# Optimization experiments

Measured on AMD Instinct MI355X. Metric: run time of the kernel, lower is better.

Reference implementation:

```python
import jax, jax.numpy as jnp
import numpy as np

N_HEAD = 16
HEAD_DIM = 64

def setup_inputs() -> dict:
    key = jax.random.key(0)
    k1, k2, k3 = jax.random.split(key, 3)
    B, S, D = 4, 2048, 1024
    x = jax.random.normal(k1, (B, S, D), dtype=jnp.float32)
    mask = jnp.tril(jnp.ones((S, S), dtype=bool))[None, None]  # (1,1,S,S) causal
    w_attn = jax.random.normal(k2, (D, 3 * D), dtype=jnp.float32) * (1.0 / np.sqrt(D))
    b_attn = jnp.zeros((3 * D,), dtype=jnp.float32)
    w_proj = jax.random.normal(k3, (D, D), dtype=jnp.float32) * (1.0 / np.sqrt(D))
    b_proj = jnp.zeros((D,), dtype=jnp.float32)
    return {"x": x, "mask": mask, "w_attn": w_attn, "b_attn": b_attn,
            "w_proj": w_proj, "b_proj": b_proj}

def reference(x, mask, w_attn, b_attn, w_proj, b_proj):
    B, S, D = x.shape
    H, hd = N_HEAD, HEAD_DIM
    qkv = x @ w_attn + b_attn                      # (B,S,3D)
    q, k, v = jnp.split(qkv, 3, axis=-1)
    q = q.reshape(B, S, H, hd).transpose(0, 2, 1, 3)  # (B,H,S,hd)
    k = k.reshape(B, S, H, hd).transpose(0, 2, 1, 3)
    v = v.reshape(B, S, H, hd).transpose(0, 2, 1, 3)
    scores = jnp.einsum('bhqd,bhkd->bhqk', q, k) / jnp.sqrt(jnp.float32(hd))
    scores = jnp.where(mask, scores, jnp.float32(-1e10))
    weights = jax.nn.softmax(scores, axis=-1)      # dropout is identity (deterministic=True)
    attn = jnp.einsum('bhqk,bhkd->bhqd', weights, v)
    attn = attn.transpose(0, 2, 1, 3).reshape(B, S, D)
    return attn @ w_proj + b_proj
```

## Files before the change

### kernel.cpp

```cpp
#include <hip/hip_runtime.h>
#include <hip/hip_bf16.h>
#include <stdint.h>


typedef uint16_t u16;
typedef __bf16 bf16x8 __attribute__((ext_vector_type(8)));
typedef __bf16 bf16x4 __attribute__((ext_vector_type(4)));
typedef short s16x4 __attribute__((ext_vector_type(4)));
typedef float f32x4 __attribute__((ext_vector_type(4)));

#define S_LEN 2048
#define DMODEL 1024
#define NHEAD 16
#define HDIM 64
#define MTOT 8192
#define NQKV 3072

__device__ __forceinline__ u16 f2bf(float f) {
    union { float f; uint32_t u; } v; v.f = f;
    uint32_t u = v.u;
    return (u16)((u + 0x7fffu + ((u >> 16) & 1u)) >> 16);
}

__device__ __forceinline__ s16x4 bits4(bf16x4 v) {
    union { bf16x4 b; s16x4 s; } u; u.b = v; return u.s;
}

__device__ __forceinline__ f32x4 mfma16(bf16x4 a, bf16x4 b, f32x4 c) {
    return __builtin_amdgcn_mfma_f32_16x16x16bf16_1k(bits4(a), bits4(b), c, 0, 0, 0);
}

__device__ __forceinline__ void async_load16(const void* g, void* l) {
    __builtin_amdgcn_global_load_lds(
        (__attribute__((address_space(1))) void*)g,
        (__attribute__((address_space(3))) void*)l,
        16, 0, 0);
}

__global__ void convert_x_kernel(const float4* __restrict__ in, ushort4* __restrict__ out, int n4) {
    int i = blockIdx.x * 256 + threadIdx.x;
    if (i < n4) {
        float4 f = in[i];
        ushort4 o;
        o.x = f2bf(f.x); o.y = f2bf(f.y); o.z = f2bf(f.z); o.w = f2bf(f.w);
        out[i] = o;
    }
}

__global__ void transpose_bf16_kernel(const float* __restrict__ in, u16* __restrict__ out, int R, int C) {
    __shared__ float tile[64][65];
    int r0 = blockIdx.y * 64, c0 = blockIdx.x * 64;
    #pragma unroll
    for (int i = 0; i < 16; ++i) {
        int idx = threadIdx.x + i * 256;
        int r = idx >> 6, c = idx & 63;
        tile[r][c] = in[(size_t)(r0 + r) * C + c0 + c];
    }
    __syncthreads();
    #pragma unroll
    for (int i = 0; i < 16; ++i) {
        int idx = threadIdx.x + i * 256;
        int c = idx >> 6, r = idx & 63;
        out[(size_t)(c0 + c) * R + r0 + r] = f2bf(tile[r][c]);
    }
}

__global__ void transpose_v_kernel(const u16* __restrict__ qkv, u16* __restrict__ vt) {
    __shared__ u16 tile[64 * 66];
    const int tid = threadIdx.x;
    const int stile = blockIdx.x, bh = blockIdx.y;
    const int b = bh >> 4, h = bh & 15;
    const u16* src = qkv + ((size_t)b * S_LEN + stile * 64) * NQKV + 2 * DMODEL + h * HDIM;
    #pragma unroll
    for (int it = 0; it < 2; ++it) {
        int item = it * 256 + tid;
        int s = item >> 3, d0 = (item & 7) * 8;
        bf16x8 v = *(const bf16x8*)(src + (size_t)s * NQKV + d0);
        const u16* vu = (const u16*)&v;
        #pragma unroll
        for (int j = 0; j < 8; ++j) tile[(d0 + j) * 66 + s] = vu[j];
    }
    __syncthreads();
    #pragma unroll
    for (int it = 0; it < 2; ++it) {
        int item = it * 256 + tid;
        int d = item >> 3, s0 = (item & 7) * 8;
        union { u16 u[8]; uint4 v; } pk;
        #pragma unroll
        for (int j = 0; j < 8; ++j) pk.u[j] = tile[d * 66 + s0 + j];
        *(uint4*)(vt + ((size_t)bh * 64 + d) * S_LEN + stile * 64 + s0) = pk.v;
    }
}

template<bool OUT_BF16>
__global__ __launch_bounds__(512, 2) void gemm256(
    const u16* __restrict__ A, const u16* __restrict__ Bt,
    const float* __restrict__ bias, void* __restrict__ C,
    int M, int N, int K)
{
    __shared__ __attribute__((aligned(16))) u16 sm[49152];
    const int tid = threadIdx.x;
    const int wave = tid >> 6, lane = tid & 63;
    const int l15 = lane & 15, q4 = lane >> 4;
    const int wm = wave & 3, wn = wave >> 2;

    const int bid = (int)blockIdx.x;
    const int xcd = bid & 7;
    const int l   = bid >> 3;
    const int MB  = M >> 8;
    const int PM  = MB >> 3;
    const int nb  = l / PM;
    const int mb  = xcd * PM + (l - nb * PM);
    const int m0 = mb << 8, n0 = nb << 7;

    const u16* Ag = A + (size_t)m0 * K;
    const u16* Bg = Bt + (size_t)n0 * K;

    const int srow = tid >> 3;
    const size_t goff0 = (size_t)srow * K + (size_t)(((tid & 7) ^ (srow & 7)) * 8);
    const size_t goff1 = goff0 + (size_t)64 * K;
    const int ldso = tid * 8;

    const int ck0 = (q4 ^ (l15 & 7)) * 8;
    const int ck1 = ((4 + q4) ^ (l15 & 7)) * 8;
    const int ra0 = (wm * 32 + l15) * 64;
    const int ra1 = ra0 + 16 * 64;
    const int rb0 = (wn * 64 + l15) * 64;

    f32x4 acc[4][4] = {};
    const int T = K >> 6;

    u16* const As = sm;
    u16* const Bs = sm + 32768;

    {
        async_load16(Ag + goff0, As + ldso);
        async_load16(Ag + goff1, As + ldso + 4096);
        async_load16(Bg + goff0, Bs + ldso);
        async_load16(Bg + goff1, Bs + ldso + 4096);
        async_load16(Ag + (size_t)128 * K + goff0, As + 8192 + ldso);
        async_load16(Ag + (size_t)128 * K + goff1, As + 8192 + ldso + 4096);
        if (T > 1) {
            async_load16(Ag + 64 + goff0, As + 2 * 8192 + ldso);
            async_load16(Ag + 64 + goff1, As + 2 * 8192 + ldso + 4096);
            async_load16(Bg + 64 + goff0, Bs + 8192 + ldso);
            async_load16(Bg + 64 + goff1, Bs + 8192 + ldso + 4096);
            asm volatile("s_waitcnt vmcnt(4)" ::: "memory");
        } else {
            asm volatile("s_waitcnt vmcnt(0)" ::: "memory");
        }
        asm volatile("s_barrier" ::: "memory");
    }

    for (int t = 0; t < T; ++t) {
        const int par = t & 1;
        const u16* As0 = As + par * 2 * 8192;
        const u16* As1 = As0 + 8192;
        const u16* Bsl = Bs + par * 8192;

        bf16x8 bfr[4][2], afr[2][2];
        #pragma unroll
        for (int nf = 0; nf < 4; ++nf) {
            bfr[nf][0] = *(const bf16x8*)(Bsl + rb0 + nf * (16 * 64) + ck0);
            bfr[nf][1] = *(const bf16x8*)(Bsl + rb0 + nf * (16 * 64) + ck1);
        }
        afr[0][0] = *(const bf16x8*)(As0 + ra0 + ck0);
        afr[0][1] = *(const bf16x8*)(As0 + ra0 + ck1);
        afr[1][0] = *(const bf16x8*)(As0 + ra1 + ck0);
        afr[1][1] = *(const bf16x8*)(As0 + ra1 + ck1);
        if (t + 1 < T) {
            const u16* g = Ag + (size_t)128 * K + (size_t)(t + 1) * 64;
            u16* l2 = As + ((par ^ 1) * 2 + 1) * 8192;
            async_load16(g + goff0, l2 + ldso);
            async_load16(g + goff1, l2 + ldso + 4096);
        }
        asm volatile("s_barrier" ::: "memory");
        __builtin_amdgcn_s_setprio(1);
        #pragma unroll
        for (int m = 0; m < 2; ++m)
            #pragma unroll
            for (int nf = 0; nf < 4; ++nf)
                #pragma unroll
                for (int kk = 0; kk < 2; ++kk)
                    acc[m][nf] = __builtin_amdgcn_mfma_f32_16x16x32_bf16(
                        afr[m][kk], bfr[nf][kk], acc[m][nf], 0, 0, 0);
        __builtin_amdgcn_s_setprio(0);
        asm volatile("s_barrier" ::: "memory");

        afr[0][0] = *(const bf16x8*)(As1 + ra0 + ck0);
        afr[0][1] = *(const bf16x8*)(As1 + ra0 + ck1);
        afr[1][0] = *(const bf16x8*)(As1 + ra1 + ck0);
        afr[1][1] = *(const bf16x8*)(As1 + ra1 + ck1);
        if (t + 2 < T) {
            const u16* ga = Ag + (size_t)(t + 2) * 64;
            const u16* gb = Bg + (size_t)(t + 2) * 64;
            u16* la = As + par * 2 * 8192;
            u16* lb = Bs + par * 8192;
            async_load16(ga + goff0, la + ldso);
            async_load16(ga + goff1, la + ldso + 4096);
            async_load16(gb + goff0, lb + ldso);
            async_load16(gb + goff1, lb + ldso + 4096);
        }
        asm volatile("s_barrier" ::: "memory");
        __builtin_amdgcn_s_setprio(1);
        #pragma unroll
        for (int m = 0; m < 2; ++m)
            #pragma unroll
            for (int nf = 0; nf < 4; ++nf)
                #pragma unroll
                for (int kk = 0; kk < 2; ++kk)
                    acc[2 + m][nf] = __builtin_amdgcn_mfma_f32_16x16x32_bf16(
                        afr[m][kk], bfr[nf][kk], acc[2 + m][nf], 0, 0, 0);
        __builtin_amdgcn_s_setprio(0);
        if (t + 1 < T) {
            if (t + 2 < T) asm volatile("s_waitcnt vmcnt(4)" ::: "memory");
            else           asm volatile("s_waitcnt vmcnt(0)" ::: "memory");
            asm volatile("s_barrier" ::: "memory");
        }
    }

    #pragma unroll
    for (int mf = 0; mf < 4; ++mf) {
        const int row = m0 + (mf >> 1) * 128 + wm * 32 + (mf & 1) * 16 + q4 * 4;
        #pragma unroll
        for (int nf = 0; nf < 4; ++nf) {
            const int col = n0 + wn * 64 + nf * 16 + l15;
            const float bv = bias[col];
            #pragma unroll
            for (int r = 0; r < 4; ++r) {
                float v = acc[mf][nf][r] + bv;
                if (OUT_BF16) ((u16*)C)[(size_t)(row + r) * N + col] = f2bf(v);
                else          ((float*)C)[(size_t)(row + r) * N + col] = v;
            }
        }
    }
}

__device__ __forceinline__ void stage_tiles(
    const u16* __restrict__ qkv, const u16* __restrict__ vt,
    size_t base, int bh, int h, int w, int srow8, int schunk,
    int kt, u16* __restrict__ KsB, u16* __restrict__ VsB)
{
    #pragma unroll
    for (int q = 0; q < 2; ++q) {
        int rloc = w * 16 + q * 8 + srow8;
        int sc = ((schunk ^ (rloc & 7)) * 8);
        async_load16(qkv + (base + (size_t)kt * 64 + rloc) * (size_t)NQKV + DMODEL + h * HDIM + sc,
                     KsB + (w * 16 + q * 8) * 64);
        async_load16(vt + ((size_t)bh * 64 + rloc) * S_LEN + kt * 64 + sc,
                     VsB + (w * 16 + q * 8) * 64);
    }
}

__device__ __forceinline__ void attn_pass(
    int qt, const u16* __restrict__ qkv, const u16* __restrict__ vt,
    __bf16* __restrict__ outb, u16 (*Ks)[64 * 64], u16 (*Vs)[64 * 64],
    int w, int lane, int bh, int h, size_t base)
{
    const int l15 = lane & 15, q4 = lane >> 4;
    const int srow8 = lane >> 3, schunk = lane & 7;

    const float QSCALE = 0.125f * 1.44269504f;
    bf16x8 qf[2][2];
    #pragma unroll
    for (int mh = 0; mh < 2; ++mh) {
        int qrow = qt * 128 + mh * 64 + w * 16 + l15;
        #pragma unroll
        for (int kc = 0; kc < 2; ++kc) {
            bf16x8 raw = *(const bf16x8*)(qkv + (base + qrow) * (size_t)NQKV + h * HDIM + kc * 32 + q4 * 8);
            bf16x8 sc;
            #pragma unroll
            for (int j = 0; j < 8; ++j) sc[j] = (__bf16)((float)raw[j] * QSCALE);
            qf[mh][kc] = sc;
        }
    }

    bf16x4 ones4;
    #pragma unroll
    for (int j = 0; j < 4; ++j) ones4[j] = (__bf16)1.0f;

    f32x4 o0[4] = {}, o1[4] = {};
    f32x4 la0 = {}, la1 = {};

    const int ktlast = 2 * qt + 1;

    __syncthreads();
    stage_tiles(qkv, vt, base, bh, h, w, srow8, schunk, 0, Ks[0], Vs[0]);
    if (ktlast >= 1)
        stage_tiles(qkv, vt, base, bh, h, w, srow8, schunk, 1, Ks[1], Vs[1]);

    for (int kt = 0; kt <= 2 * qt; ++kt) {
        const int buf = kt % 3;
        __syncthreads();
        int pf = kt + 2;
        if (pf <= ktlast)
            stage_tiles(qkv, vt, base, bh, h, w, srow8, schunk, pf, Ks[pf % 3], Vs[pf % 3]);

        f32x4 st0[4] = {}, st1[4] = {};
        #pragma unroll
        for (int nt = 0; nt < 4; ++nt) {
            int n = nt * 16 + l15;
            #pragma unroll
            for (int kc = 0; kc < 2; ++kc) {
                int ch = (((kc * 4 + q4) ^ (n & 7)) * 8);
                bf16x8 kf = *(const bf16x8*)(&Ks[buf][n * 64 + ch]);
                st0[nt] = __builtin_amdgcn_mfma_f32_16x16x32_bf16(kf, qf[0][kc], st0[nt], 0, 0, 0);
                st1[nt] = __builtin_amdgcn_mfma_f32_16x16x32_bf16(kf, qf[1][kc], st1[nt], 0, 0, 0);
            }
        }

        if (kt == 2 * qt) {
            #pragma unroll
            for (int nt = 0; nt < 4; ++nt)
                #pragma unroll
                for (int r = 0; r < 4; ++r) {
                    int keyl = nt * 16 + q4 * 4 + r;
                    if (keyl > w * 16 + l15) st0[nt][r] = -1e30f;
                }
        }

        bf16x4 pb0[4], pb1[4];
        #pragma unroll
        for (int nt = 0; nt < 4; ++nt)
            #pragma unroll
            for (int r = 0; r < 4; ++r) {
                pb0[nt][r] = (__bf16)__builtin_amdgcn_exp2f(st0[nt][r]);
                pb1[nt][r] = (__bf16)__builtin_amdgcn_exp2f(st1[nt][r]);
            }

        #pragma unroll
        for (int nt = 0; nt < 4; ++nt) {
            #pragma unroll
            for (int mt = 0; mt < 4; ++mt) {
                int row = mt * 16 + l15;
                int ch = (nt * 2 + (q4 >> 1)) ^ (row & 7);
                bf16x4 vf = *(const bf16x4*)(&Vs[buf][row * 64 + ch * 8 + (q4 & 1) * 4]);
                o0[mt] = mfma16(vf, pb0[nt], o0[mt]);
                o1[mt] = mfma16(vf, pb1[nt], o1[mt]);
            }
            la0 = mfma16(ones4, pb0[nt], la0);
            la1 = mfma16(ones4, pb1[nt], la1);
        }
    }

    {
        const int buf = ktlast % 3;
        __syncthreads();

        f32x4 st1[4] = {};
        #pragma unroll
        for (int nt = 0; nt < 4; ++nt) {
            int n = nt * 16 + l15;
            #pragma unroll
            for (int kc = 0; kc < 2; ++kc) {
                int ch = (((kc * 4 + q4) ^ (n & 7)) * 8);
                bf16x8 kf = *(const bf16x8*)(&Ks[buf][n * 64 + ch]);
                st1[nt] = __builtin_amdgcn_mfma_f32_16x16x32_bf16(kf, qf[1][kc], st1[nt], 0, 0, 0);
            }
        }
        bf16x4 pb1[4];
        #pragma unroll
        for (int nt = 0; nt < 4; ++nt)
            #pragma unroll
            for (int r = 0; r < 4; ++r) {
                int keyl = nt * 16 + q4 * 4 + r;
                float s = (keyl > w * 16 + l15) ? -1e30f : st1[nt][r];
                pb1[nt][r] = (__bf16)__builtin_amdgcn_exp2f(s);
            }
        #pragma unroll
        for (int nt = 0; nt < 4; ++nt) {
            #pragma unroll
            for (int mt = 0; mt < 4; ++mt) {
                int row = mt * 16 + l15;
                int ch = (nt * 2 + (q4 >> 1)) ^ (row & 7);
                bf16x4 vf = *(const bf16x4*)(&Vs[buf][row * 64 + ch * 8 + (q4 & 1) * 4]);
                o1[mt] = mfma16(vf, pb1[nt], o1[mt]);
            }
            la1 = mfma16(ones4, pb1[nt], la1);
        }
    }

    float inv0 = 1.0f / la0[0], inv1 = 1.0f / la1[0];
    int row0 = qt * 128 + w * 16 + l15;
    int row1 = row0 + 64;
    #pragma unroll
    for (int mt = 0; mt < 4; ++mt) {
        union { __bf16 b[4]; ushort4 v; } p0, p1;
        #pragma unroll
        for (int r = 0; r < 4; ++r) {
            p0.b[r] = (__bf16)(o0[mt][r] * inv0);
            p1.b[r] = (__bf16)(o1[mt][r] * inv1);
        }
        int col = h * HDIM + mt * 16 + q4 * 4;
        *(ushort4*)(&outb[(base + row0) * (size_t)DMODEL + col]) = p0.v;
        *(ushort4*)(&outb[(base + row1) * (size_t)DMODEL + col]) = p1.v;
    }
}

__global__ __launch_bounds__(256, 3) void attn_kernel(
    const u16* __restrict__ qkv, const u16* __restrict__ vt, u16* __restrict__ out)
{
    __shared__ __attribute__((aligned(16))) u16 Ks[3][64 * 64];
    __shared__ __attribute__((aligned(16))) u16 Vs[3][64 * 64];

    const int tid = threadIdx.x;
    const int w = tid >> 6, lane = tid & 63;
    const int bh = blockIdx.y;
    const int b = bh >> 4, h = bh & 15;
    const size_t base = (size_t)b * S_LEN;
    const int NT = (int)gridDim.x * 2;

    attn_pass(NT - 1 - (int)blockIdx.x, qkv, vt, (__bf16*)out, Ks, Vs, w, lane, bh, h, base);
    attn_pass((int)blockIdx.x,          qkv, vt, (__bf16*)out, Ks, Vs, w, lane, bh, h, base);
}

extern "C" void kernel_launch(void* const* d_in, const int* in_sizes, int n_in,
                              void* d_out, int out_size, void* d_ws, size_t ws_size,
                              hipStream_t stream) {
    const float* x      = (const float*)d_in[0];
    const float* w_attn = (const float*)d_in[2];
    const float* b_attn = (const float*)d_in[3];
    const float* w_proj = (const float*)d_in[4];
    const float* b_proj = (const float*)d_in[5];

    u16* xb   = (u16*)d_ws;
    u16* wat  = xb  + (size_t)MTOT * DMODEL;
    u16* wpt  = wat + (size_t)NQKV * DMODEL;
    u16* qkv  = wpt + (size_t)DMODEL * DMODEL;
    u16* attn = qkv + (size_t)MTOT * NQKV;
    u16* vt   = xb;

    convert_x_kernel<<<(MTOT * DMODEL / 4 + 255) / 256, 256, 0, stream>>>(
        (const float4*)x, (ushort4*)xb, MTOT * DMODEL / 4);
    transpose_bf16_kernel<<<dim3(NQKV / 64, DMODEL / 64), 256, 0, stream>>>(w_attn, wat, DMODEL, NQKV);
    transpose_bf16_kernel<<<dim3(DMODEL / 64, DMODEL / 64), 256, 0, stream>>>(w_proj, wpt, DMODEL, DMODEL);

    gemm256<true><<<dim3((MTOT / 256) * (NQKV / 128)), 512, 0, stream>>>(
        xb, wat, b_attn, (void*)qkv, MTOT, NQKV, DMODEL);

    transpose_v_kernel<<<dim3(S_LEN / 64, 4 * NHEAD), 256, 0, stream>>>(qkv, vt);

    attn_kernel<<<dim3(S_LEN / 256, 4 * NHEAD), 256, 0, stream>>>(qkv, vt, attn);

    gemm256<false><<<dim3((MTOT / 256) * (DMODEL / 128)), 512, 0, stream>>>(
        attn, wpt, b_proj, d_out, MTOT, DMODEL, DMODEL);
}
```

Before: 267.7 us.

## Enlarge GEMM block tile to 256x256 with four-phase A/B staging

The bf16 GEMM goes from a 256x128 block tile to a square 256x256 tile. Each wave now covers 128x64 with 32 accumulators instead of 16, and B is double-buffered across two 128-row halves, with A/B prefetch split over four MFMA phases per k-step. The goal is more data reuse per loaded byte and less global/LDS traffic per FLOP. The trade-off is half as many blocks (fewer for the projection GEMM: 128 blocks on 256 CUs), 128KB of LDS, and higher register pressure under launch_bounds(512,2).

After: 278.7 us. 4.1% more time.

```diff
diff --git a/kernel.cpp b/kernel.cpp
--- a/kernel.cpp
+++ b/kernel.cpp
@@ -93,25 +93,28 @@
 }
 
 template<bool OUT_BF16>
-__global__ __launch_bounds__(512, 2) void gemm256(
+__global__ __launch_bounds__(512, 2) void gemm256sq(
     const u16* __restrict__ A, const u16* __restrict__ Bt,
     const float* __restrict__ bias, void* __restrict__ C,
     int M, int N, int K)
 {
-    __shared__ __attribute__((aligned(16))) u16 sm[49152];
+    __shared__ __attribute__((aligned(16))) u16 sm[65536];
+    u16* const As = sm;
+    u16* const Bs = sm + 32768;
+
     const int tid = threadIdx.x;
     const int wave = tid >> 6, lane = tid & 63;
     const int l15 = lane & 15, q4 = lane >> 4;
-    const int wm = wave & 3, wn = wave >> 2;
+    const int wm = wave >> 2, wn = wave & 3;
 
     const int bid = (int)blockIdx.x;
     const int xcd = bid & 7;
-    const int l   = bid >> 3;
+    const int lx  = bid >> 3;
     const int MB  = M >> 8;
     const int PM  = MB >> 3;
-    const int nb  = l / PM;
-    const int mb  = xcd * PM + (l - nb * PM);
-    const int m0 = mb << 8, n0 = nb << 7;
+    const int nb  = lx / PM;
+    const int mb  = xcd * PM + (lx - nb * PM);
+    const int m0 = mb << 8, n0 = nb << 8;
 
     const u16* Ag = A + (size_t)m0 * K;
     const u16* Bg = Bt + (size_t)n0 * K;
@@ -123,95 +126,85 @@
 
     const int ck0 = (q4 ^ (l15 & 7)) * 8;
     const int ck1 = ((4 + q4) ^ (l15 & 7)) * 8;
-    const int ra0 = (wm * 32 + l15) * 64;
-    const int ra1 = ra0 + 16 * 64;
     const int rb0 = (wn * 64 + l15) * 64;
 
-    f32x4 acc[4][4] = {};
+    f32x4 acc[8][4] = {};
     const int T = K >> 6;
 
-    u16* const As = sm;
-    u16* const Bs = sm + 32768;
-
-    {
-        async_load16(Ag + goff0, As + ldso);
-        async_load16(Ag + goff1, As + ldso + 4096);
-        async_load16(Bg + goff0, Bs + ldso);
-        async_load16(Bg + goff1, Bs + ldso + 4096);
-        async_load16(Ag + (size_t)128 * K + goff0, As + 8192 + ldso);
-        async_load16(Ag + (size_t)128 * K + goff1, As + 8192 + ldso + 4096);
-        if (T > 1) {
-            async_load16(Ag + 64 + goff0, As + 2 * 8192 + ldso);
-            async_load16(Ag + 64 + goff1, As + 2 * 8192 + ldso + 4096);
-            async_load16(Bg + 64 + goff0, Bs + 8192 + ldso);
-            async_load16(Bg + 64 + goff1, Bs + 8192 + ldso + 4096);
-            asm volatile("s_waitcnt vmcnt(4)" ::: "memory");
-        } else {
-            asm volatile("s_waitcnt vmcnt(0)" ::: "memory");
-        }
-        asm volatile("s_barrier" ::: "memory");
-    }
+#define STAGE_A(t_, h_) do { \
+    const u16* g_ = Ag + (size_t)(h_) * 128 * K + (size_t)(t_) * 64; \
+    u16* d_ = As + (((t_) & 1) * 2 + (h_)) * 8192; \
+    async_load16(g_ + goff0, d_ + ldso); \
+    async_load16(g_ + goff1, d_ + ldso + 4096); \
+} while (0)
+
+#define STAGE_B(t_, h_) do { \
+    const u16* g_ = Bg + (size_t)(h_) * 128 * K + (size_t)(t_) * 64; \
+    u16* d_ = Bs + ((t_) & 1) * 16384 + (h_) * 8192; \
+    async_load16(g_ + goff0, d_ + ldso); \
+    async_load16(g_ + goff1, d_ + ldso + 4096); \
+} while (0)
+
+#define LOAD_AF(P_) do { \
+    af[0][0] = *(const bf16x8*)(Ah + ((2 * (P_)) * 16 + l15) * 64 + ck0); \
+    af[0][1] = *(const bf16x8*)(Ah + ((2 * (P_)) * 16 + l15) * 64 + ck1); \
+    af[1][0] = *(const bf16x8*)(Ah + ((2 * (P_) + 1) * 16 + l15) * 64 + ck0); \
+    af[1][1] = *(const bf16x8*)(Ah + ((2 * (P_) + 1) * 16 + l15) * 64 + ck1); \
+} while (0)
+
+#define PHASE_MFMA(P_) do { \
+    asm volatile("s_barrier" ::: "memory"); \
+    __builtin_amdgcn_s_setprio(1); \
+    _Pragma("unroll") \
+    for (int i_ = 0; i_ < 2; ++i_) \
+        _Pragma("unroll") \
+        for (int nf_ = 0; nf_ < 4; ++nf_) \
+            _Pragma("unroll") \
+            for (int kk_ = 0; kk_ < 2; ++kk_) \
+                acc[2 * (P_) + i_][nf_] = __builtin_amdgcn_mfma_f32_16x16x32_bf16( \
+                    af[i_][kk_], bfr[nf_][kk_], acc[2 * (P_) + i_][nf_], 0, 0, 0); \
+    __builtin_amdgcn_s_setprio(0); \
+} while (0)
+
+    STAGE_A(0, 0); STAGE_A(0, 1); STAGE_B(0, 0); STAGE_B(0, 1);
+    if (T > 1) {
+        STAGE_B(1, 0); STAGE_B(1, 1);
+        asm volatile("s_waitcnt vmcnt(4)" ::: "memory");
+    } else {
+        asm volatile("s_waitcnt vmcnt(0)" ::: "memory");
+    }
+    asm volatile("s_barrier" ::: "memory");
 
     for (int t = 0; t < T; ++t) {
         const int par = t & 1;
-        const u16* As0 = As + par * 2 * 8192;
-        const u16* As1 = As0 + 8192;
-        const u16* Bsl = Bs + par * 8192;
-
-        bf16x8 bfr[4][2], afr[2][2];
+        const u16* Ah = As + (par * 2 + wm) * 8192;
+        const u16* Bl = Bs + par * 16384;
+
+        bf16x8 af[2][2], bfr[4][2];
+
         #pragma unroll
         for (int nf = 0; nf < 4; ++nf) {
-            bfr[nf][0] = *(const bf16x8*)(Bsl + rb0 + nf * (16 * 64) + ck0);
-            bfr[nf][1] = *(const bf16x8*)(Bsl + rb0 + nf * (16 * 64) + ck1);
-        }
-        afr[0][0] = *(const bf16x8*)(As0 + ra0 + ck0);
-        afr[0][1] = *(const bf16x8*)(As0 + ra0 + ck1);
-        afr[1][0] = *(const bf16x8*)(As0 + ra1 + ck0);
-        afr[1][1] = *(const bf16x8*)(As0 + ra1 + ck1);
-        if (t + 1 < T) {
-            const u16* g = Ag + (size_t)128 * K + (size_t)(t + 1) * 64;
-            u16* l2 = As + ((par ^ 1) * 2 + 1) * 8192;
-            async_load16(g + goff0, l2 + ldso);
-            async_load16(g + goff1, l2 + ldso + 4096);
-        }
+            bfr[nf][0] = *(const bf16x8*)(Bl + rb0 + nf * (16 * 64) + ck0);
+            bfr[nf][1] = *(const bf16x8*)(Bl + rb0 + nf * (16 * 64) + ck1);
+        }
+        LOAD_AF(0);
+        if (t + 1 < T) STAGE_A(t + 1, 0);
+        PHASE_MFMA(0);
         asm volatile("s_barrier" ::: "memory");
-        __builtin_amdgcn_s_setprio(1);
-        #pragma unroll
-        for (int m = 0; m < 2; ++m)
-            #pragma unroll
-            for (int nf = 0; nf < 4; ++nf)
-                #pragma unroll
-                for (int kk = 0; kk < 2; ++kk)
-                    acc[m][nf] = __builtin_amdgcn_mfma_f32_16x16x32_bf16(
-                        afr[m][kk], bfr[nf][kk], acc[m][nf], 0, 0, 0);
-        __builtin_amdgcn_s_setprio(0);
+
+        LOAD_AF(1);
+        if (t + 1 < T) STAGE_A(t + 1, 1);
+        PHASE_MFMA(1);
         asm volatile("s_barrier" ::: "memory");
 
-        afr[0][0] = *(const bf16x8*)(As1 + ra0 + ck0);
-        afr[0][1] = *(const bf16x8*)(As1 + ra0 + ck1);
-        afr[1][0] = *(const bf16x8*)(As1 + ra1 + ck0);
-        afr[1][1] = *(const bf16x8*)(As1 + ra1 + ck1);
-        if (t + 2 < T) {
-            const u16* ga = Ag + (size_t)(t + 2) * 64;
-            const u16* gb = Bg + (size_t)(t + 2) * 64;
-            u16* la = As + par * 2 * 8192;
-            u16* lb = Bs + par * 8192;
-            async_load16(ga + goff0, la + ldso);
-            async_load16(ga + goff1, la + ldso + 4096);
-            async_load16(gb + goff0, lb + ldso);
-            async_load16(gb + goff1, lb + ldso + 4096);
-        }
+        LOAD_AF(2);
+        if (t + 2 < T) STAGE_B(t + 2, 0);
+        PHASE_MFMA(2);
         asm volatile("s_barrier" ::: "memory");
-        __builtin_amdgcn_s_setprio(1);
-        #pragma unroll
-        for (int m = 0; m < 2; ++m)
-            #pragma unroll
-            for (int nf = 0; nf < 4; ++nf)
-                #pragma unroll
-                for (int kk = 0; kk < 2; ++kk)
-                    acc[2 + m][nf] = __builtin_amdgcn_mfma_f32_16x16x32_bf16(
-                        afr[m][kk], bfr[nf][kk], acc[2 + m][nf], 0, 0, 0);
-        __builtin_amdgcn_s_setprio(0);
+
+        LOAD_AF(3);
+        if (t + 2 < T) STAGE_B(t + 2, 1);
+        PHASE_MFMA(3);
         if (t + 1 < T) {
             if (t + 2 < T) asm volatile("s_waitcnt vmcnt(4)" ::: "memory");
             else           asm volatile("s_waitcnt vmcnt(0)" ::: "memory");
@@ -219,9 +212,14 @@
         }
     }
 
-    #pragma unroll
-    for (int mf = 0; mf < 4; ++mf) {
-        const int row = m0 + (mf >> 1) * 128 + wm * 32 + (mf & 1) * 16 + q4 * 4;
+#undef STAGE_A
+#undef STAGE_B
+#undef LOAD_AF
+#undef PHASE_MFMA
+
+    #pragma unroll
+    for (int mf = 0; mf < 8; ++mf) {
+        const int row = m0 + wm * 128 + mf * 16 + q4 * 4;
         #pragma unroll
         for (int nf = 0; nf < 4; ++nf) {
             const int col = n0 + wn * 64 + nf * 16 + l15;
@@ -435,13 +433,13 @@
     transpose_bf16_kernel<<<dim3(NQKV / 64, DMODEL / 64), 256, 0, stream>>>(w_attn, wat, DMODEL, NQKV);
     transpose_bf16_kernel<<<dim3(DMODEL / 64, DMODEL / 64), 256, 0, stream>>>(w_proj, wpt, DMODEL, DMODEL);
 
-    gemm256<true><<<dim3((MTOT / 256) * (NQKV / 128)), 512, 0, stream>>>(
+    gemm256sq<true><<<dim3((MTOT / 256) * (NQKV / 256)), 512, 0, stream>>>(
         xb, wat, b_attn, (void*)qkv, MTOT, NQKV, DMODEL);
 
     transpose_v_kernel<<<dim3(S_LEN / 64, 4 * NHEAD), 256, 0, stream>>>(qkv, vt);
 
     attn_kernel<<<dim3(S_LEN / 256, 4 * NHEAD), 256, 0, stream>>>(qkv, vt, attn);
 
-    gemm256<false><<<dim3((MTOT / 256) * (DMODEL / 128)), 512, 0, stream>>>(
+    gemm256sq<false><<<dim3((MTOT / 256) * (DMODEL / 256)), 512, 0, stream>>>(
         attn, wpt, b_proj, d_out, MTOT, DMODEL, DMODEL);
 }
```
